# Kernel optimization log

Measured on AMD Instinct MI355X. Metric: run time of the kernel, lower is better.

## Reference

```python
import jax, jax.numpy as jnp
import numpy as np

KH, KW = 3, 3
PAD = 1
C_IN, C_OUT = 64, 128


def unfold(x, kh, kw, pad):
    # x: (B, C, H, W) -> (B, C, kh*kw, H*W), torch.nn.functional.unfold ordering
    B, C, H, W = x.shape
    xp = jnp.pad(x, ((0, 0), (0, 0), (pad, pad), (pad, pad)))
    patches = jnp.stack(
        [xp[:, :, i:i + H, j:j + W] for i in range(kh) for j in range(kw)],
        axis=2,
    )  # (B, C, K, H, W)
    return patches.reshape(B, C, kh * kw, H * W)


def setup_inputs() -> dict:
    key = jax.random.key(0)
    k1, k2, k3 = jax.random.split(key, 3)
    B, H, W = 8, 128, 128
    inp = jax.random.normal(k1, (B, C_IN, H, W), dtype=jnp.float32)
    g_buffer = jax.random.uniform(k2, (B, 2, H, W), dtype=jnp.float32)
    # weights param as in torch: (1, C*kh*kw, 1, out_channels), kaiming-uniform-ish
    wdepth = C_IN * KH * KW
    bound = float(np.sqrt(6.0 / wdepth))
    weights = jax.random.uniform(k3, (1, wdepth, 1, C_OUT), dtype=jnp.float32,
                                 minval=-bound, maxval=bound)
    bias = jnp.zeros((C_OUT,), dtype=jnp.float32)
    return {"input": inp, "g_buffer": g_buffer, "weights": weights, "bias": bias}


def reference(input, g_buffer, weights, bias):
    B, C, H, W = input.shape
    K = KH * KW
    L = H * W
    depth = 2.0 * (g_buffer[:, -1:, :, :] - 0.5)  # (B, 1, H, W)

    input_unf = unfold(input, KH, KW, PAD)          # (B, C, K, L)
    depth_unf = unfold(depth, KH, KW, PAD)          # (B, 1, K, L)

    # bilateral depth weighting
    dfeat = depth_unf - depth.reshape(B, 1, 1, L)   # (B, 1, K, L)
    dfeat = jnp.sum(dfeat * dfeat, axis=1)          # (B, K, L)
    wf = jnp.exp(-dfeat)
    wf = 9.0 * wf / jnp.sum(wf, axis=1, keepdims=True)  # (B, K, L)

    filt = input_unf * wf[:, None, :, :]            # (B, C, K, L)
    filt = filt.reshape(B, C * K, L)

    W2 = weights.reshape(C_OUT, C * K)              # raw reshape, matches torch .view
    out_unf = jnp.einsum('bkl,ok->bol', filt, W2)   # (B, C_OUT, L)
    out = out_unf.reshape(B, C_OUT, H, W) + bias[None, :, None, None]
    return out
```

## Files before the change

kernel.cpp:

```cpp
#include <hip/hip_runtime.h>
#include <hip/hip_bf16.h>
#include <stdint.h>

typedef _Float16 f16x8 __attribute__((ext_vector_type(8)));
typedef float    f32x4 __attribute__((ext_vector_type(4)));

#define CIN   64
#define COUT  128
#define HH    128
#define WW    128
#define BB    8

#define TROW  130
#define ROWBYTES (130 * 128)
#define TSIZE ((size_t)BB * TROW * ROWBYTES)

#define LROWB (34 * 128)
#define NCHKT (4 * 272)

#define AS1 __attribute__((address_space(1)))
#define AS3 __attribute__((address_space(3)))


__global__ void prep_plus(const float* __restrict__ wflat, _Float16* __restrict__ bp,
                          _Float16* __restrict__ T) {
    int gid = blockIdx.x * 256 + threadIdx.x;
    if (gid < 8 * 18 * 64 * 8) {
        int j = gid & 7;
        int l = (gid >> 3) & 63;
        int s = (gid >> 9) % 18;
        int n = gid / (18 * 512);
        int o = n * 16 + (l & 15);
        int c = ((s & 1) << 5) + ((l >> 4) << 3) + j;
        int k = s >> 1;
        bp[gid] = (_Float16)wflat[o * 576 + c * 9 + k];
        return;
    }
    int h = gid - 8 * 18 * 64 * 8;
    if (h < 16 * 1040) {
        int row = h / 1040, c = h - row * 1040;
        int b = row >> 1, yp = (row & 1) * 129;
        f16x8 z = {};
        *(f16x8*)((char*)T + (size_t)(b * TROW + yp) * ROWBYTES + c * 16) = z;
    }
}

__global__ __launch_bounds__(256) void transpose_pass(const float* __restrict__ inp,
                                                      _Float16* __restrict__ T) {
    __shared__ float sT[64][129];
    const int b   = blockIdx.x >> 7;
    const int y   = blockIdx.x & 127;
    const int tid = threadIdx.x;

    const float* ib = inp + ((long)b * CIN * HH + y) * WW;
    const int xq = tid & 31, c8 = tid >> 5;
    #pragma unroll
    for (int i = 0; i < 8; ++i) {
        int c = c8 * 8 + i;
        float4 v = *(const float4*)(ib + (long)c * (HH * WW) + (xq << 2));
        *(float4*)&sT[c][xq << 2] = v;
    }
    __syncthreads();

    const int x  = tid & 127;
    const int ch = tid >> 7;
    char* rowp = (char*)T + (size_t)(b * TROW + y + 1) * ROWBYTES + (size_t)(x + 1) * 128;
    const int sw = (x + 1) & 7;
    for (int c0 = ch * 8; c0 < 64; c0 += 16) {
        f16x8 v;
        #pragma unroll
        for (int j = 0; j < 8; ++j) v[j] = (_Float16)sT[c0 + j][x];
        *(f16x8*)(rowp + (((c0 >> 3) ^ sw) << 4)) = v;
    }
    if (tid < 16) {
        char* basep = (char*)T + (size_t)(b * TROW + y + 1) * ROWBYTES
                    + ((tid >> 3) ? 129 * 128 : 0) + (tid & 7) * 16;
        f16x8 z = {};
        *(f16x8*)basep = z;
    }
}

__global__ __launch_bounds__(256, 3) void depthcnn_main(
    const _Float16* __restrict__ T, const float* __restrict__ gbuf,
    const float* __restrict__ bias, const _Float16* __restrict__ aprep,
    float* __restrict__ out)
{
    __shared__ __align__(1024) char sIn[4 * LROWB];
    __shared__ _Float16 sWf[2][32][16];

    const int blk    = blockIdx.x;
    const int b      = blk & 7;
    const int rest   = blk >> 3;
    const int strip  = rest & 63;
    const int xq     = rest >> 6;
    const int ystart = strip << 1;
    const int x0     = xq << 5;

    const int tid  = threadIdx.x;
    const int wave = tid >> 6;
    const int lane = tid & 63;
    const int oi   = wave;
    const int l15  = lane & 15;
    const int g4   = lane >> 4;

    {
        const char* Tb = (const char*)T + ((size_t)b * TROW + ystart) * ROWBYTES
                       + (size_t)x0 * 128;
        #pragma unroll
        for (int tt = 0; tt < 5; ++tt) {
            int t = tt * 256 + tid;
            if (t < NCHKT) {
                int tr = t / 272, c = t - tr * 272;
                __builtin_amdgcn_global_load_lds(
                    (const AS1 uint32_t*)(Tb + (size_t)tr * ROWBYTES + c * 16),
                    (AS3 uint32_t*)(sIn + tr * LROWB + c * 16), 16, 0, 0);
            }
        }
    }

    if (tid < 64) {
        const int r = tid >> 5, pxl = tid & 31, x = x0 + pxl, y = ystart + r;
        const float* g = gbuf + ((size_t)b * 2 + 1) * (HH * WW);
        float dc = 2.f * (g[y * WW + x] - 0.5f);
        float e[9];
        float ssum = 0.f;
        #pragma unroll
        for (int k = 0; k < 9; ++k) {
            int yy = y + (k / 3) - 1;
            int xx = x + (k % 3) - 1;
            float dn = 0.f;
            if ((unsigned)yy < 128u && (unsigned)xx < 128u)
                dn = 2.f * (g[yy * WW + xx] - 0.5f);
            float df = dn - dc;
            float ek = __expf(-df * df);
            e[k] = ek;
            ssum += ek;
        }
        float sc = 9.f / ssum;
        #pragma unroll
        for (int k = 0; k < 9; ++k) sWf[r][pxl][k] = (_Float16)(e[k] * sc);
    }

    float bv[2][4];
    #pragma unroll
    for (int t2 = 0; t2 < 2; ++t2)
        #pragma unroll
        for (int r4 = 0; r4 < 4; ++r4)
            bv[t2][r4] = bias[(oi << 5) + (t2 << 4) + (g4 << 2) + r4];

    __syncthreads();

    f16x8    w07[2][2];
    _Float16 w8s[2][2];
    #pragma unroll
    for (int r = 0; r < 2; ++r)
        #pragma unroll
        for (int pt = 0; pt < 2; ++pt) {
            const int pxl = (pt << 4) + l15;
            w07[r][pt] = *(const f16x8*)&sWf[r][pxl][0];
            w8s[r][pt] = sWf[r][pxl][8];
        }

    f32x4 acc[2][2][2];
    #pragma unroll
    for (int r = 0; r < 2; ++r)
        #pragma unroll
        for (int t2 = 0; t2 < 2; ++t2)
            #pragma unroll
            for (int pt = 0; pt < 2; ++pt)
                acc[r][t2][pt] = (f32x4){0.f, 0.f, 0.f, 0.f};

    const f16x8* __restrict__ ap = (const f16x8*)aprep;

    #pragma unroll
    for (int half = 0; half < 2; ++half) {
        f16x8 afr[2][9];
        #pragma unroll
        for (int t2 = 0; t2 < 2; ++t2) {
            const int ot = (oi << 1) + t2;
            #pragma unroll
            for (int ss = 0; ss < 9; ++ss)
                afr[t2][ss] = ap[(size_t)(ot * 18 + half * 9 + ss) * 64 + lane];
        }
        __builtin_amdgcn_sched_barrier(0);

        #pragma unroll
        for (int r = 0; r < 2; ++r) {
            #pragma unroll
            for (int ss = 0; ss < 9; ++ss) {
                const int s  = half * 9 + ss;
                const int k  = s >> 1;
                const int ch = s & 1;
                const int dy = k / 3;
                const int dx = k - 3 * dy;
                f16x8 bf[2];
                #pragma unroll
                for (int pt = 0; pt < 2; ++pt) {
                    const int xl  = (pt << 4) + l15 + dx;
                    const int off = (r + dy) * LROWB + (xl << 7)
                                  + ((((ch << 2) | g4) ^ (xl & 7)) << 4);
                    f16x8 iv = *(const f16x8*)(sIn + off);
                    _Float16 wh = (k < 8) ? w07[r][pt][k] : w8s[r][pt];
                    f16x8 w8 = {wh, wh, wh, wh, wh, wh, wh, wh};
                    bf[pt] = iv * w8;
                }
                #pragma unroll
                for (int t2 = 0; t2 < 2; ++t2)
                    #pragma unroll
                    for (int pt = 0; pt < 2; ++pt)
                        acc[r][t2][pt] = __builtin_amdgcn_mfma_f32_16x16x32_f16(
                            afr[t2][ss], bf[pt], acc[r][t2][pt], 0, 0, 0);
            }
        }
    }

    float* ob = out + (size_t)b * COUT * (HH * WW) + x0;
    #pragma unroll
    for (int r = 0; r < 2; ++r) {
        const int y = ystart + r;
        #pragma unroll
        for (int t2 = 0; t2 < 2; ++t2) {
            #pragma unroll
            for (int pt = 0; pt < 2; ++pt) {
                #pragma unroll
                for (int r4 = 0; r4 < 4; ++r4) {
                    const int o = (oi << 5) + (t2 << 4) + (g4 << 2) + r4;
                    ob[(size_t)o * (HH * WW) + (size_t)y * WW + (pt << 4) + l15]
                        = acc[r][t2][pt][r4] + bv[t2][r4];
                }
            }
        }
    }
}

extern "C" void kernel_launch(void* const* d_in, const int* in_sizes, int n_in,
                              void* d_out, int out_size, void* d_ws, size_t ws_size,
                              hipStream_t stream) {
    const float* inp  = (const float*)d_in[0];
    const float* gbuf = (const float*)d_in[1];
    const float* wts  = (const float*)d_in[2];
    const float* bias = (const float*)d_in[3];

    _Float16* T  = (_Float16*)d_ws;
    _Float16* bp = (_Float16*)((char*)d_ws + TSIZE);

    hipLaunchKernelGGL(prep_plus, dim3(353), dim3(256), 0, stream, wts, bp, T);
    hipLaunchKernelGGL(transpose_pass, dim3(BB * HH), dim3(256), 0, stream, inp, T);
    hipLaunchKernelGGL(depthcnn_main, dim3(2048), dim3(256), 0, stream,
                       T, gbuf, bias, bp, (float*)d_out);
}
```

Measured before the change: 49.82 us.

## Cut register pressure with double-buffered weight fragments and LDS depth weights

Replaces the bulk preload of 18 weight fragments per half with a two-stage double buffer that loads the next kernel tap's fragments while the current tap computes. Depth weights are stored tap-major in LDS and read per tap instead of held in registers, and the bias is loaded at store time instead of preloaded. Launch bounds are raised from 3 to 4 blocks per SM. This lowers the register count to allow higher occupancy. In exchange the MFMA loop waits more often on global and LDS loads, and there is less room to hide that latency.

```diff
diff --git a/kernel.cpp b/kernel.cpp
--- a/kernel.cpp
+++ b/kernel.cpp
@@ -80,13 +80,13 @@
     }
 }
 
-__global__ __launch_bounds__(256, 3) void depthcnn_main(
+__global__ __launch_bounds__(256, 4) void depthcnn_main(
     const _Float16* __restrict__ T, const float* __restrict__ gbuf,
     const float* __restrict__ bias, const _Float16* __restrict__ aprep,
     float* __restrict__ out)
 {
     __shared__ __align__(1024) char sIn[4 * LROWB];
-    __shared__ _Float16 sWf[2][32][16];
+    __shared__ _Float16 sWf[2][9][36];
 
     const int blk    = blockIdx.x;
     const int b      = blk & 7;
@@ -138,28 +138,10 @@
         }
         float sc = 9.f / ssum;
         #pragma unroll
-        for (int k = 0; k < 9; ++k) sWf[r][pxl][k] = (_Float16)(e[k] * sc);
-    }
-
-    float bv[2][4];
-    #pragma unroll
-    for (int t2 = 0; t2 < 2; ++t2)
-        #pragma unroll
-        for (int r4 = 0; r4 < 4; ++r4)
-            bv[t2][r4] = bias[(oi << 5) + (t2 << 4) + (g4 << 2) + r4];
+        for (int k = 0; k < 9; ++k) sWf[r][k][pxl] = (_Float16)(e[k] * sc);
+    }
 
     __syncthreads();
-
-    f16x8    w07[2][2];
-    _Float16 w8s[2][2];
-    #pragma unroll
-    for (int r = 0; r < 2; ++r)
-        #pragma unroll
-        for (int pt = 0; pt < 2; ++pt) {
-            const int pxl = (pt << 4) + l15;
-            w07[r][pt] = *(const f16x8*)&sWf[r][pxl][0];
-            w8s[r][pt] = sWf[r][pxl][8];
-        }
 
     f32x4 acc[2][2][2];
     #pragma unroll
@@ -172,27 +154,33 @@
 
     const f16x8* __restrict__ ap = (const f16x8*)aprep;
 
-    #pragma unroll
-    for (int half = 0; half < 2; ++half) {
-        f16x8 afr[2][9];
-        #pragma unroll
-        for (int t2 = 0; t2 < 2; ++t2) {
-            const int ot = (oi << 1) + t2;
-            #pragma unroll
-            for (int ss = 0; ss < 9; ++ss)
-                afr[t2][ss] = ap[(size_t)(ot * 18 + half * 9 + ss) * 64 + lane];
-        }
-        __builtin_amdgcn_sched_barrier(0);
-
+    f16x8 af[2][2][2];
+    #pragma unroll
+    for (int t2 = 0; t2 < 2; ++t2)
+        #pragma unroll
+        for (int ch = 0; ch < 2; ++ch)
+            af[0][t2][ch] = ap[(size_t)(((oi * 2 + t2) * 18) + ch) * 64 + lane];
+
+    #pragma unroll
+    for (int k = 0; k < 9; ++k) {
+        if (k < 8) {
+            #pragma unroll
+            for (int t2 = 0; t2 < 2; ++t2)
+                #pragma unroll
+                for (int ch = 0; ch < 2; ++ch)
+                    af[(k + 1) & 1][t2][ch] =
+                        ap[(size_t)(((oi * 2 + t2) * 18) + 2 * (k + 1) + ch) * 64 + lane];
+        }
+        const int dy = k / 3;
+        const int dx = k - 3 * dy;
         #pragma unroll
         for (int r = 0; r < 2; ++r) {
-            #pragma unroll
-            for (int ss = 0; ss < 9; ++ss) {
-                const int s  = half * 9 + ss;
-                const int k  = s >> 1;
-                const int ch = s & 1;
-                const int dy = k / 3;
-                const int dx = k - 3 * dy;
+            _Float16 wh[2];
+            #pragma unroll
+            for (int pt = 0; pt < 2; ++pt)
+                wh[pt] = sWf[r][k][(pt << 4) + l15];
+            #pragma unroll
+            for (int ch = 0; ch < 2; ++ch) {
                 f16x8 bf[2];
                 #pragma unroll
                 for (int pt = 0; pt < 2; ++pt) {
@@ -200,8 +188,8 @@
                     const int off = (r + dy) * LROWB + (xl << 7)
                                   + ((((ch << 2) | g4) ^ (xl & 7)) << 4);
                     f16x8 iv = *(const f16x8*)(sIn + off);
-                    _Float16 wh = (k < 8) ? w07[r][pt][k] : w8s[r][pt];
-                    f16x8 w8 = {wh, wh, wh, wh, wh, wh, wh, wh};
+                    f16x8 w8 = {wh[pt], wh[pt], wh[pt], wh[pt],
+                                wh[pt], wh[pt], wh[pt], wh[pt]};
                     bf[pt] = iv * w8;
                 }
                 #pragma unroll
@@ -209,7 +197,7 @@
                     #pragma unroll
                     for (int pt = 0; pt < 2; ++pt)
                         acc[r][t2][pt] = __builtin_amdgcn_mfma_f32_16x16x32_f16(
-                            afr[t2][ss], bf[pt], acc[r][t2][pt], 0, 0, 0);
+                            af[k & 1][t2][ch], bf[pt], acc[r][t2][pt], 0, 0, 0);
             }
         }
     }
@@ -226,7 +214,7 @@
                 for (int r4 = 0; r4 < 4; ++r4) {
                     const int o = (oi << 5) + (t2 << 4) + (g4 << 2) + r4;
                     ob[(size_t)o * (HH * WW) + (size_t)y * WW + (pt << 4) + l15]
-                        = acc[r][t2][pt][r4] + bv[t2][r4];
+                        = acc[r][t2][pt][r4] + bias[o];
                 }
             }
         }
```

New measurement: 50.31 us. Within noise of the previous version (+1.0%).
